# Optimization experiments

Measured on AMD Instinct MI355X. Metric: run time of the kernel, lower is better.

The kernel has to match this reference:

```python
import jax, jax.numpy as jnp
import numpy as np

FP8_MAX = 448.0


def setup_inputs() -> dict:
    key = jax.random.key(0)
    kx, kw = jax.random.split(key)
    in_features, out_features = 1024, 1024
    x = jax.random.normal(kx, (32768, in_features), dtype=jnp.float32)
    # kaiming_uniform_ with a=sqrt(5): bound = sqrt(6/((1+a^2)*fan_in)) = sqrt(1/fan_in)
    bound = 1.0 / np.sqrt(in_features)
    weight = jax.random.uniform(kw, (out_features, in_features), dtype=jnp.float32,
                                minval=-bound, maxval=bound)
    bias = jnp.zeros((out_features,), dtype=jnp.float32)
    return {"x": x, "weight": weight, "bias": bias}


def reference(x, weight, bias):
    # per-tensor input quant
    input_scale = jnp.maximum(jnp.max(jnp.abs(x)) / FP8_MAX, 1e-12)
    x_q = jnp.round(jnp.clip(x / input_scale, -FP8_MAX, FP8_MAX))
    # per-output-channel weight quant
    weight_amax = jnp.max(jnp.abs(weight), axis=1)            # [out]
    weight_scale = jnp.maximum(weight_amax / FP8_MAX, 1e-12)  # [out]
    weight_q = jnp.round(jnp.clip(weight / weight_scale[:, None], -FP8_MAX, FP8_MAX))
    # integer-valued GEMM in fp32, then dequant + bias
    output_q = jnp.einsum('ti,oi->to', x_q, weight_q)          # [T, out]
    output = output_q * (input_scale * weight_scale)[None, :]
    return output + bias
```

## Files before the change

kernel.cpp:

```cpp
#include <hip/hip_runtime.h>
#include <hip/hip_fp16.h>

#define FP8_MAX 448.0f
#define M_ 32768
#define N_ 1024
#define K_ 1024
#define BM 128
#define BN 128
#define BK 64

typedef _Float16 f16x8 __attribute__((ext_vector_type(8)));
typedef _Float16 f16x4 __attribute__((ext_vector_type(4)));
typedef __fp16  h16x2 __attribute__((ext_vector_type(2)));
typedef float f32x16 __attribute__((ext_vector_type(16)));

__device__ inline void gload_lds16(const void* g, void* l) {
    __builtin_amdgcn_global_load_lds(
        (const __attribute__((address_space(1))) void*)g,
        (__attribute__((address_space(3))) void*)l,
        16, 0, 0);
}

__global__ __launch_bounds__(256) void prep_kernel(const float* __restrict__ x,
                                                   const float* __restrict__ w,
                                                   float* __restrict__ xamax_part,
                                                   float* __restrict__ wscale,
                                                   _Float16* __restrict__ wq,
                                                   int n) {
    __shared__ float sm[4];
    if (blockIdx.x < 1024) {
        int row = blockIdx.x;
        const float4* wr4 = (const float4*)(w + (size_t)row * K_);
        float4 v = wr4[threadIdx.x];
        float m = fmaxf(fmaxf(fabsf(v.x), fabsf(v.y)), fmaxf(fabsf(v.z), fabsf(v.w)));
        #pragma unroll
        for (int off = 32; off > 0; off >>= 1)
            m = fmaxf(m, __shfl_down(m, off, 64));
        if ((threadIdx.x & 63) == 0) sm[threadIdx.x >> 6] = m;
        __syncthreads();
        m = fmaxf(fmaxf(sm[0], sm[1]), fmaxf(sm[2], sm[3]));
        float scale = fmaxf(m / FP8_MAX, 1e-12f);
        if (threadIdx.x == 0) wscale[row] = scale;
        float inv = 1.0f / scale;
        f16x4 o;
        o[0] = (_Float16)rintf(fminf(fmaxf(v.x * inv, -FP8_MAX), FP8_MAX));
        o[1] = (_Float16)rintf(fminf(fmaxf(v.y * inv, -FP8_MAX), FP8_MAX));
        o[2] = (_Float16)rintf(fminf(fmaxf(v.z * inv, -FP8_MAX), FP8_MAX));
        o[3] = (_Float16)rintf(fminf(fmaxf(v.w * inv, -FP8_MAX), FP8_MAX));
        ((f16x4*)(wq + (size_t)row * K_))[threadIdx.x] = o;
    } else {
        float m = 0.0f;
        const float4* x4 = (const float4*)x;
        int n4 = n >> 2;
        int stride = 2048 * 256;
        for (int i = (blockIdx.x - 1024) * 256 + threadIdx.x; i < n4; i += stride) {
            float4 v = x4[i];
            m = fmaxf(m, fmaxf(fmaxf(fabsf(v.x), fabsf(v.y)),
                               fmaxf(fabsf(v.z), fabsf(v.w))));
        }
        #pragma unroll
        for (int off = 32; off > 0; off >>= 1)
            m = fmaxf(m, __shfl_down(m, off, 64));
        if ((threadIdx.x & 63) == 0) sm[threadIdx.x >> 6] = m;
        __syncthreads();
        if (threadIdx.x == 0) {
            xamax_part[blockIdx.x - 1024] =
                fmaxf(fmaxf(sm[0], sm[1]), fmaxf(sm[2], sm[3]));
        }
    }
}

__global__ __launch_bounds__(256) void gemm_kernel(const float* __restrict__ x,
                                                   const _Float16* __restrict__ wq,
                                                   const float* __restrict__ xamax_part,
                                                   const float* __restrict__ wscale,
                                                   const float* __restrict__ bias,
                                                   float* __restrict__ out) {
    __shared__ __align__(16) _Float16 sA[BM * BK];
    __shared__ __align__(16) _Float16 sB[BN * BK];

    const int tid = threadIdx.x;

    const float4* p4 = (const float4*)xamax_part;
    float4 pa = p4[tid];
    float4 pb = p4[tid + 256];
    float m = fmaxf(fmaxf(fmaxf(pa.x, pa.y), fmaxf(pa.z, pa.w)),
                    fmaxf(fmaxf(pb.x, pb.y), fmaxf(pb.z, pb.w)));
    #pragma unroll
    for (int off = 32; off > 0; off >>= 1)
        m = fmaxf(m, __shfl_down(m, off, 64));
    float* red = (float*)sA;
    if ((tid & 63) == 0) red[tid >> 6] = m;
    __syncthreads();
    const float amax = fmaxf(fmaxf(red[0], red[1]), fmaxf(red[2], red[3]));
    __syncthreads();
    const float iscale = fmaxf(amax / FP8_MAX, 1e-12f);
    const float inv = 1.0f / iscale;

    const int wave = tid >> 6;
    const int lane = tid & 63;
    const int h   = lane >> 5;
    const int m32 = lane & 31;
    const int m7  = m32 & 7;
    const int wm = (wave >> 1) * 64;
    const int wn = (wave & 1) * 64;

    const int m0 = (int)(blockIdx.x & 255) * BM;
    const int n0 = (int)(blockIdx.x >> 8) * BN;

    const int trow = tid >> 3;
    const int tcol = (((tid & 7) ^ (trow & 7)) * 8);
    const _Float16* Bg = wq + ((size_t)(n0 + trow)) * K_ + tcol;
    char* lB = (char*)sB + wave * 1024;

    const int arow = tid >> 3;
    const int ach  = tid & 7;
    const float* Ag = x + (size_t)(m0 + arow) * K_ + ach * 8;
    _Float16* Aw = sA + (size_t)arow * BK + ((ach ^ (arow & 7)) * 8);

    f32x16 acc[2][2] = {};

    for (int kt = 0; kt < K_; kt += BK) {
        #pragma unroll
        for (int rr = 0; rr < 4; ++rr)
            gload_lds16(Bg + kt + (size_t)(rr * 32) * K_, lB + rr * 4096);
        #pragma unroll
        for (int rr = 0; rr < 4; ++rr) {
            const float* src = Ag + kt + (size_t)(rr * 32) * K_;
            float4 v0 = *(const float4*)src;
            float4 v1 = *(const float4*)(src + 4);
            h16x2 t0 = __builtin_amdgcn_cvt_pkrtz(rintf(v0.x * inv), rintf(v0.y * inv));
            h16x2 t1 = __builtin_amdgcn_cvt_pkrtz(rintf(v0.z * inv), rintf(v0.w * inv));
            h16x2 t2 = __builtin_amdgcn_cvt_pkrtz(rintf(v1.x * inv), rintf(v1.y * inv));
            h16x2 t3 = __builtin_amdgcn_cvt_pkrtz(rintf(v1.z * inv), rintf(v1.w * inv));
            f16x8 q;
            q[0] = (_Float16)t0[0]; q[1] = (_Float16)t0[1];
            q[2] = (_Float16)t1[0]; q[3] = (_Float16)t1[1];
            q[4] = (_Float16)t2[0]; q[5] = (_Float16)t2[1];
            q[6] = (_Float16)t3[0]; q[7] = (_Float16)t3[1];
            *(f16x8*)(Aw + (size_t)(rr * 32) * BK) = q;
        }
        __syncthreads();
        #pragma unroll
        for (int ks = 0; ks < 4; ++ks) {
            f16x8 a[2], b[2];
            const int chunk = ks * 2 + h;
            const int pos = (chunk ^ m7) * 8;
            #pragma unroll
            for (int i = 0; i < 2; ++i)
                a[i] = *(const f16x8*)&sA[(wm + i * 32 + m32) * BK + pos];
            #pragma unroll
            for (int j = 0; j < 2; ++j)
                b[j] = *(const f16x8*)&sB[(wn + j * 32 + m32) * BK + pos];
            #pragma unroll
            for (int i = 0; i < 2; ++i)
                #pragma unroll
                for (int j = 0; j < 2; ++j)
                    acc[i][j] = __builtin_amdgcn_mfma_f32_32x32x16_f16(a[i], b[j], acc[i][j], 0, 0, 0);
        }
        __syncthreads();
    }

    #pragma unroll
    for (int j = 0; j < 2; ++j) {
        int col = n0 + wn + j * 32 + m32;
        float sc = iscale * wscale[col];
        float bs = bias[col];
        #pragma unroll
        for (int i = 0; i < 2; ++i) {
            int rb = m0 + wm + i * 32 + 4 * h;
            #pragma unroll
            for (int reg = 0; reg < 16; ++reg) {
                int row = rb + (reg & 3) + 8 * (reg >> 2);
                out[(size_t)row * N_ + col] = acc[i][j][reg] * sc + bs;
            }
        }
    }
}

extern "C" void kernel_launch(void* const* d_in, const int* in_sizes, int n_in,
                              void* d_out, int out_size, void* d_ws, size_t ws_size,
                              hipStream_t stream) {
    const float* x    = (const float*)d_in[0];
    const float* w    = (const float*)d_in[1];
    const float* bias = (const float*)d_in[2];
    float* out = (float*)d_out;

    char* ws = (char*)d_ws;
    float* xamax_part  = (float*)(ws + 1024);
    float* wscale      = (float*)(ws + 16384);
    _Float16* wq       = (_Float16*)(ws + 32768);

    prep_kernel<<<3072, 256, 0, stream>>>(x, w, xamax_part, wscale, wq, M_ * K_);
    gemm_kernel<<<2048, 256, 0, stream>>>(x, wq, xamax_part, wscale, bias, out);
}
```

Measured before the change: 368.2 us.

## Prefetch next A tile into registers with double-buffered LDS and remap block order

Loads the next K-slice of fp32 activations into registers before the MFMA loop, then quantizes and writes it into a second A buffer in LDS after compute. This hides global load latency for A behind the MFMA work. The block index mapping also changes to group 8 M-tiles by 8 N-tiles, so concurrently running blocks share x and weight tiles in cache. The costs are more registers (32 prefetched floats per thread), double the A LDS, and one wasted wraparound load on the last iteration.

Result: faster. 316.9 us (-13.9%).

```diff
diff --git a/kernel.cpp b/kernel.cpp
--- a/kernel.cpp
+++ b/kernel.cpp
@@ -19,6 +19,19 @@
         (const __attribute__((address_space(1))) void*)g,
         (__attribute__((address_space(3))) void*)l,
         16, 0, 0);
+}
+
+__device__ inline f16x8 quant8(float4 v0, float4 v1, float inv) {
+    h16x2 t0 = __builtin_amdgcn_cvt_pkrtz(rintf(v0.x * inv), rintf(v0.y * inv));
+    h16x2 t1 = __builtin_amdgcn_cvt_pkrtz(rintf(v0.z * inv), rintf(v0.w * inv));
+    h16x2 t2 = __builtin_amdgcn_cvt_pkrtz(rintf(v1.x * inv), rintf(v1.y * inv));
+    h16x2 t3 = __builtin_amdgcn_cvt_pkrtz(rintf(v1.z * inv), rintf(v1.w * inv));
+    f16x8 q;
+    q[0] = (_Float16)t0[0]; q[1] = (_Float16)t0[1];
+    q[2] = (_Float16)t1[0]; q[3] = (_Float16)t1[1];
+    q[4] = (_Float16)t2[0]; q[5] = (_Float16)t2[1];
+    q[6] = (_Float16)t3[0]; q[7] = (_Float16)t3[1];
+    return q;
 }
 
 __global__ __launch_bounds__(256) void prep_kernel(const float* __restrict__ x,
@@ -76,7 +89,7 @@
                                                    const float* __restrict__ wscale,
                                                    const float* __restrict__ bias,
                                                    float* __restrict__ out) {
-    __shared__ __align__(16) _Float16 sA[BM * BK];
+    __shared__ __align__(16) _Float16 sA[2][BM * BK];
     __shared__ __align__(16) _Float16 sB[BN * BK];
 
     const int tid = threadIdx.x;
@@ -105,8 +118,9 @@
     const int wm = (wave >> 1) * 64;
     const int wn = (wave & 1) * 64;
 
-    const int m0 = (int)(blockIdx.x & 255) * BM;
-    const int n0 = (int)(blockIdx.x >> 8) * BN;
+    const int bb = (int)blockIdx.x;
+    const int n0 = (((bb >> 3) & 7)) * BN;
+    const int m0 = (((bb >> 6) << 3) + (bb & 7)) * BM;
 
     const int trow = tid >> 3;
     const int tcol = (((tid & 7) ^ (trow & 7)) * 8);
@@ -116,31 +130,36 @@
     const int arow = tid >> 3;
     const int ach  = tid & 7;
     const float* Ag = x + (size_t)(m0 + arow) * K_ + ach * 8;
-    _Float16* Aw = sA + (size_t)arow * BK + ((ach ^ (arow & 7)) * 8);
+    _Float16* Aw0 = (_Float16*)sA + (size_t)arow * BK + ((ach ^ (arow & 7)) * 8);
 
     f32x16 acc[2][2] = {};
-
+    float4 pv[4][2];
+
+    #pragma unroll
+    for (int rr = 0; rr < 4; ++rr) {
+        const float* src = Ag + (size_t)(rr * 32) * K_;
+        pv[rr][0] = *(const float4*)src;
+        pv[rr][1] = *(const float4*)(src + 4);
+    }
+    #pragma unroll
+    for (int rr = 0; rr < 4; ++rr)
+        *(f16x8*)(Aw0 + (size_t)(rr * 32) * BK) = quant8(pv[rr][0], pv[rr][1], inv);
+
+    int buf = 0;
     for (int kt = 0; kt < K_; kt += BK) {
         #pragma unroll
         for (int rr = 0; rr < 4; ++rr)
             gload_lds16(Bg + kt + (size_t)(rr * 32) * K_, lB + rr * 4096);
+        const int kn = (kt + BK) & (K_ - 1);
         #pragma unroll
         for (int rr = 0; rr < 4; ++rr) {
-            const float* src = Ag + kt + (size_t)(rr * 32) * K_;
-            float4 v0 = *(const float4*)src;
-            float4 v1 = *(const float4*)(src + 4);
-            h16x2 t0 = __builtin_amdgcn_cvt_pkrtz(rintf(v0.x * inv), rintf(v0.y * inv));
-            h16x2 t1 = __builtin_amdgcn_cvt_pkrtz(rintf(v0.z * inv), rintf(v0.w * inv));
-            h16x2 t2 = __builtin_amdgcn_cvt_pkrtz(rintf(v1.x * inv), rintf(v1.y * inv));
-            h16x2 t3 = __builtin_amdgcn_cvt_pkrtz(rintf(v1.z * inv), rintf(v1.w * inv));
-            f16x8 q;
-            q[0] = (_Float16)t0[0]; q[1] = (_Float16)t0[1];
-            q[2] = (_Float16)t1[0]; q[3] = (_Float16)t1[1];
-            q[4] = (_Float16)t2[0]; q[5] = (_Float16)t2[1];
-            q[6] = (_Float16)t3[0]; q[7] = (_Float16)t3[1];
-            *(f16x8*)(Aw + (size_t)(rr * 32) * BK) = q;
-        }
-        __syncthreads();
+            const float* src = Ag + kn + (size_t)(rr * 32) * K_;
+            pv[rr][0] = *(const float4*)src;
+            pv[rr][1] = *(const float4*)(src + 4);
+        }
+        __syncthreads();
+
+        const _Float16* sAb = (const _Float16*)sA + (size_t)buf * (BM * BK);
         #pragma unroll
         for (int ks = 0; ks < 4; ++ks) {
             f16x8 a[2], b[2];
@@ -148,7 +167,7 @@
             const int pos = (chunk ^ m7) * 8;
             #pragma unroll
             for (int i = 0; i < 2; ++i)
-                a[i] = *(const f16x8*)&sA[(wm + i * 32 + m32) * BK + pos];
+                a[i] = *(const f16x8*)&sAb[(wm + i * 32 + m32) * BK + pos];
             #pragma unroll
             for (int j = 0; j < 2; ++j)
                 b[j] = *(const f16x8*)&sB[(wn + j * 32 + m32) * BK + pos];
@@ -159,6 +178,14 @@
                     acc[i][j] = __builtin_amdgcn_mfma_f32_32x32x16_f16(a[i], b[j], acc[i][j], 0, 0, 0);
         }
         __syncthreads();
+
+        if (kt + BK < K_) {
+            _Float16* Awn = Aw0 + (size_t)(buf ^ 1) * (BM * BK);
+            #pragma unroll
+            for (int rr = 0; rr < 4; ++rr)
+                *(f16x8*)(Awn + (size_t)(rr * 32) * BK) = quant8(pv[rr][0], pv[rr][1], inv);
+            buf ^= 1;
+        }
     }
 
     #pragma unroll
```
